# Kernel optimization log

Measured on AMD Instinct MI355X. Metric: run time of the kernel, lower is better.

## Reference

```python
import jax, jax.numpy as jnp
import numpy as np
from jax import lax

B, L, C, P = 512, 6, 4, 45

def _conv(x, w, b, pad):
    y = lax.conv_general_dilated(x, w, (1, 1), [(pad, pad), (pad, pad)],
                                 dimension_numbers=('NCHW', 'OIHW', 'NCHW'))
    return y + b[None, :, None, None]

def _maxpool2(x):
    return lax.reduce_window(x, -jnp.inf, lax.max, (1, 1, 2, 2), (1, 1, 2, 2), 'VALID')

def _prelu(x, a):
    return jnp.where(x >= 0, x, a * x)

def setup_inputs() -> dict:
    key = jax.random.key(0)
    ks = jax.random.split(key, 16)
    s = 0.05
    inp = {
        'x': jax.random.normal(ks[0], (B, L, C, P, P), jnp.float32),
        'w0': jax.random.normal(ks[1], (32, C, 5, 5), jnp.float32) * s,
        'b0': jnp.zeros((32,), jnp.float32),
        'w1': jax.random.normal(ks[2], (32, 32, 5, 5), jnp.float32) * s,
        'b1': jnp.zeros((32,), jnp.float32),
        'w2': jax.random.normal(ks[3], (64, 32, 4, 4), jnp.float32) * s,
        'b2': jnp.zeros((64,), jnp.float32),
        'w3': jax.random.normal(ks[4], (64, 64, 3, 3), jnp.float32) * s,
        'b3': jnp.zeros((64,), jnp.float32),
        'a0': jnp.float32(0.25), 'a1': jnp.float32(0.25),
        'a2': jnp.float32(0.25), 'a3': jnp.float32(0.25),
        'fc1_w': jax.random.normal(ks[5], (L, 256, 128), jnp.float32) * s,
        'fc1_b': jnp.zeros((L, 128), jnp.float32),
        'a4': jnp.full((L, 1), 0.25, jnp.float32),
        'fc2_w': jax.random.normal(ks[6], (L, 128, 64), jnp.float32) * s,
        'fc2_b': jnp.zeros((L, 64), jnp.float32),
        'a5': jnp.full((L, 1), 0.25, jnp.float32),
        'fc3_w': jax.random.normal(ks[7], (L, 64, 4), jnp.float32) * s,
        'fc3_b': jnp.zeros((L, 4), jnp.float32),
    }
    return inp

def reference(x, w0, b0, w1, b1, w2, b2, w3, b3, a0, a1, a2, a3,
              fc1_w, fc1_b, a4, fc2_w, fc2_b, a5, fc3_w, fc3_b):
    b, l = x.shape[0], x.shape[1]
    # Conv tower shares weights across landmarks -> fold landmark into batch.
    h = x.reshape(b * l, x.shape[2], P, P)
    h = _maxpool2(_prelu(_conv(h, w0, b0, 1), a0))   # (BL,32,21,21)
    h = _maxpool2(_prelu(_conv(h, w1, b1, 1), a1))   # (BL,32,9,9)
    h = _maxpool2(_prelu(_conv(h, w2, b2, 1), a2))   # (BL,64,4,4)
    h = _prelu(_conv(h, w3, b3, 0), a3)              # (BL,64,2,2)
    h = h.reshape(b, l, 256)
    # Per-landmark FC heads as batched GEMMs.
    h = _prelu(jnp.einsum('bli,lio->blo', h, fc1_w) + fc1_b, a4)
    h = _prelu(jnp.einsum('bli,lio->blo', h, fc2_w) + fc2_b, a5)
    out = jnp.einsum('bli,lio->blo', h, fc3_w) + fc3_b   # (B,L,4)
    return out
```

## Files before the change

kernel.cpp:

```cpp
#include <hip/hip_runtime.h>
#include <stdint.h>

typedef _Float16 f16;
typedef _Float16 half8 __attribute__((ext_vector_type(8)));
typedef _Float16 half4 __attribute__((ext_vector_type(4)));
typedef float floatx16 __attribute__((ext_vector_type(16)));

#define NIMG 3072

#define WS_W0T   0
#define WS_W1T   10240
#define WS_W2T   61440
#define WS_W3T   126976
#define WS_FC1T  200704
#define WS_FC2T  593920
#define WS_FC3T  692224
#define WS_H2    720896
#define WS_H3F   16646144

#define Z16 {0.f,0.f,0.f,0.f,0.f,0.f,0.f,0.f,0.f,0.f,0.f,0.f,0.f,0.f,0.f,0.f}

__global__ __launch_bounds__(256) void k_prep(
    const float* __restrict__ w0, const float* __restrict__ w1, const float* __restrict__ w2,
    const float* __restrict__ w3, const float* __restrict__ fc1w, const float* __restrict__ fc2w,
    const float* __restrict__ fc3w,
    f16* __restrict__ w0t, f16* __restrict__ w1t, f16* __restrict__ w2t, f16* __restrict__ w3t,
    f16* __restrict__ fc1t, f16* __restrict__ fc2t, f16* __restrict__ fc3t)
{
  int stride = gridDim.x * blockDim.x;
  int g0 = blockIdx.x * blockDim.x + threadIdx.x;
  for (int i = g0; i < 5120; i += stride) {
    int j = i & 7, co = (i >> 3) & 31, hf = (i >> 8) & 1, ch = (i >> 9) & 1, ky = i >> 10;
    int k = ch * 16 + hf * 8 + j;
    f16 v = (f16)0.f;
    if (k < 20) { int kx = k >> 2, ci = k & 3; v = (f16)w0[((co * 4 + ci) * 5 + ky) * 5 + kx]; }
    w0t[i] = v;
  }
  for (int i = g0; i < 25600; i += stride) {
    int j = i & 7, co = (i >> 3) & 31, hf = (i >> 8) & 1, ch = (i >> 9) & 1, tap = i >> 10;
    int ci = ch * 16 + hf * 8 + j, ky = tap / 5, kx = tap % 5;
    w1t[i] = (f16)w1[((co * 32 + ci) * 5 + ky) * 5 + kx];
  }
  for (int i = g0; i < 32768; i += stride) {
    int j = i & 7, co = (i >> 3) & 31, hf = (i >> 8) & 1, ct = (i >> 9) & 1, ch = (i >> 10) & 1, tap = i >> 11;
    int ci = ch * 16 + hf * 8 + j, cog = ct * 32 + co, ky = tap >> 2, kx = tap & 3;
    w2t[i] = (f16)w2[((cog * 32 + ci) * 4 + ky) * 4 + kx];
  }
  for (int i = g0; i < 36864; i += stride) {
    int j = i & 7, col = (i >> 3) & 31, hf = (i >> 8) & 1, ct = (i >> 9) & 1, c = i >> 10;
    int k = c * 16 + hf * 8 + j, tap = k >> 6, ci = k & 63, co = ct * 32 + col;
    int ky = tap / 3, kx = tap % 3;
    w3t[i] = (f16)w3[((co * 64 + ci) * 3 + ky) * 3 + kx];
  }
  for (int i = g0; i < 196608; i += stride) {
    int j = i & 7, col = (i >> 3) & 31, hf = (i >> 8) & 1, nt = (i >> 9) & 3, c = (i >> 11) & 15, l = i >> 15;
    int k = c * 16 + hf * 8 + j, o = nt * 32 + col;
    fc1t[i] = (f16)fc1w[(l * 256 + k) * 128 + o];
  }
  for (int i = g0; i < 49152; i += stride) {
    int j = i & 7, col = (i >> 3) & 31, hf = (i >> 8) & 1, nt = (i >> 9) & 1, c = (i >> 10) & 7, l = i >> 13;
    int k = c * 16 + hf * 8 + j, o = nt * 32 + col;
    fc2t[i] = (f16)fc2w[(l * 128 + k) * 64 + o];
  }
  for (int i = g0; i < 12288; i += stride) {
    int j = i & 7, col = (i >> 3) & 31, hf = (i >> 8) & 1, c = (i >> 9) & 3, l = i >> 11;
    int k = c * 16 + hf * 8 + j;
    f16 v = (f16)0.f;
    if (col < 4) v = (f16)fc3w[(l * 64 + k) * 4 + col];
    fc3t[i] = v;
  }
}

__global__ __launch_bounds__(512) void k_conv01(
    const float* __restrict__ x,
    const f16* __restrict__ w0t, const float* __restrict__ b0, const float* __restrict__ a0p,
    const f16* __restrict__ w1t, const float* __restrict__ b1, const float* __restrict__ a1p,
    f16* __restrict__ h2g)
{
  __shared__ __align__(16) uint32_t smem_u[16328];
  f16* sh   = (f16*)smem_u;
  f16* s_x  = sh;
  f16* s_h1 = sh + 9776;

  const int n = blockIdx.x, tid = threadIdx.x;
  const int wv = tid >> 6, l = tid & 63;
  const int hf = l >> 5, m = l & 31, dr = m >> 3, dc = m & 7, col = m;
  const float a0 = a0p[0], a1 = a1p[0];
  const float b0c = b0[col], b1c = b1[col];
  const half8* w0t8 = (const half8*)w0t;
  const half8* w1t8 = (const half8*)w1t;

  for (int i = tid; i < 16328; i += 512) smem_u[i] = 0u;
  __syncthreads();
  const float* xin = x + n * 8100;
  for (int i = tid; i < 8100; i += 512) {
    int ci = i / 2025, r = i % 2025;
    int y = r / 45, xx = r % 45;
    s_x[((y + 1) * 52 + (xx + 1)) * 4 + ci] = (f16)xin[i];
  }
  __syncthreads();

  half8 B0[5][2];
  #pragma unroll
  for (int ky = 0; ky < 5; ++ky)
    #pragma unroll
    for (int ch = 0; ch < 2; ++ch)
      B0[ky][ch] = w0t8[(ky * 2 + ch) * 64 + hf * 32 + col];

  const int r0lut0[11] = {0,4,8,12,16,20,24,28,32,36,38};
  for (int t = wv; t < 66; t += 8) {
    int r0 = r0lut0[t / 6], cb = (t % 6) * 8;
    int rowb = r0 + dr, colb = cb + dc;
    const f16* pA0 = s_x + (rowb * 52 + colb + 2 * hf) * 4;
    const f16* pA1 = s_x + (rowb * 52 + colb + 4) * 4;
    floatx16 acc = Z16;
    #pragma unroll
    for (int ky = 0; ky < 5; ++ky) {
      half4 lo = *(const half4*)(pA0 + ky * 208);
      half4 hi = *(const half4*)(pA0 + ky * 208 + 4);
      half8 a0v = __builtin_shufflevector(lo, hi, 0,1,2,3,4,5,6,7);
      acc = __builtin_amdgcn_mfma_f32_32x32x16_f16(a0v, B0[ky][0], acc, 0, 0, 0);
      half8 a1v = {(f16)0,(f16)0,(f16)0,(f16)0,(f16)0,(f16)0,(f16)0,(f16)0};
      if (hf == 0) {
        half4 l1 = *(const half4*)(pA1 + ky * 208);
        a1v[0] = l1[0]; a1v[1] = l1[1]; a1v[2] = l1[2]; a1v[3] = l1[3];
      }
      acc = __builtin_amdgcn_mfma_f32_32x32x16_f16(a1v, B0[ky][1], acc, 0, 0, 0);
    }
    #pragma unroll
    for (int pp = 0; pp < 2; ++pp)
      #pragma unroll
      for (int c2 = 0; c2 < 2; ++c2) {
        float v = fmaxf(fmaxf(acc[8*pp + 2*c2], acc[8*pp + 2*c2 + 1]),
                        fmaxf(acc[8*pp + 4 + 2*c2], acc[8*pp + 4 + 2*c2 + 1]));
        v += b0c; v = (v >= 0.f) ? v : a0 * v;
        int pr = (r0 >> 1) + pp, pc = (cb >> 1) + 2 * hf + c2;
        if (pc < 21) s_h1[((pr + 1) * 26 + (pc + 1)) * 40 + col] = (f16)v;
      }
  }
  __syncthreads();

  const int r0lut1[5] = {0, 4, 8, 12, 14};
  const int cclut[3]  = {0, 8, 14};
  int t0 = wv * 2;
  int t1 = t0 + 1; if (t1 > 14) t1 = 14;
  int r0a = r0lut1[t0 / 3], cca = cclut[t0 % 3];
  int r0b = r0lut1[t1 / 3], ccb = cclut[t1 % 3];
  const f16* pAa = s_h1 + ((r0a + dr) * 26 + cca + dc) * 40 + hf * 8;
  const f16* pAb = s_h1 + ((r0b + dr) * 26 + ccb + dc) * 40 + hf * 8;
  floatx16 accA = Z16;
  floatx16 accB = Z16;
  for (int ky = 0; ky < 5; ++ky) {
    const half8* wb = w1t8 + ky * 640 + hf * 32 + col;
    const f16* qa = pAa + ky * 1040;
    const f16* qb = pAb + ky * 1040;
    #pragma unroll
    for (int kx = 0; kx < 5; ++kx) {
      #pragma unroll
      for (int ch = 0; ch < 2; ++ch) {
        half8 b  = wb[kx * 128 + ch * 64];
        half8 aA = *(const half8*)(qa + kx * 40 + ch * 16);
        half8 aB = *(const half8*)(qb + kx * 40 + ch * 16);
        accA = __builtin_amdgcn_mfma_f32_32x32x16_f16(aA, b, accA, 0, 0, 0);
        accB = __builtin_amdgcn_mfma_f32_32x32x16_f16(aB, b, accB, 0, 0, 0);
      }
    }
  }
  f16* outp = h2g + n * 2592;
  #pragma unroll
  for (int tt = 0; tt < 2; ++tt) {
    const floatx16 acc = tt ? accB : accA;
    int r0 = tt ? r0b : r0a, cc = tt ? ccb : cca;
    #pragma unroll
    for (int pp = 0; pp < 2; ++pp)
      #pragma unroll
      for (int c2 = 0; c2 < 2; ++c2) {
        float v = fmaxf(fmaxf(acc[8*pp + 2*c2], acc[8*pp + 2*c2 + 1]),
                        fmaxf(acc[8*pp + 4 + 2*c2], acc[8*pp + 4 + 2*c2 + 1]));
        v += b1c; v = (v >= 0.f) ? v : a1 * v;
        int pr = (r0 >> 1) + pp, pc = (cc >> 1) + 2 * hf + c2;
        if (pc < 9) outp[(pr * 9 + pc) * 32 + col] = (f16)v;
      }
  }
}

__global__ __launch_bounds__(256) void k_conv2(
    const f16* __restrict__ h2g, const f16* __restrict__ w2t,
    const float* __restrict__ b2, const float* __restrict__ a2p,
    f16* __restrict__ h3f)
{
  __shared__ __align__(16) uint32_t s_u[5760];
  f16* s2 = (f16*)s_u;
  const int n0 = blockIdx.x * 2, tid = threadIdx.x;
  const int wv = tid >> 6, l = tid & 63;
  const int hf = l >> 5, m = l & 31, dr = m >> 3, dc = m & 7, col = m;
  const int img = wv >> 1, ct = wv & 1;
  const float a2 = a2p[0];
  const float b2c = b2[ct * 32 + col];
  const half8* w2t8 = (const half8*)w2t;

  for (int i = tid; i < 5760; i += 256) s_u[i] = 0u;
  __syncthreads();
  for (int c = tid; c < 648; c += 256) {
    int im = c / 324, rr = c % 324, pos = rr >> 2, part = rr & 3;
    int r = pos / 9, cc = pos % 9;
    *(half8*)(s2 + im * 5760 + ((r + 1) * 12 + (cc + 1)) * 40 + part * 8) =
      *(const half8*)(h2g + (n0 + im) * 2592 + pos * 32 + part * 8);
  }
  __syncthreads();

  const f16* sbase = s2 + img * 5760;
  const f16* pA0 = sbase + (dr * 12 + dc) * 40 + hf * 8;
  const f16* pA4 = sbase + ((4 + dr) * 12 + dc) * 40 + hf * 8;
  floatx16 acc0 = Z16;
  floatx16 acc4 = Z16;
  for (int tap = 0; tap < 16; ++tap) {
    int ky = tap >> 2, kx = tap & 3;
    int aoff = (ky * 12 + kx) * 40;
    #pragma unroll
    for (int ch = 0; ch < 2; ++ch) {
      half8 b  = w2t8[tap * 256 + ch * 128 + ct * 64 + hf * 32 + col];
      half8 a0 = *(const half8*)(pA0 + aoff + ch * 16);
      half8 a4 = *(const half8*)(pA4 + aoff + ch * 16);
      acc0 = __builtin_amdgcn_mfma_f32_32x32x16_f16(a0, b, acc0, 0, 0, 0);
      acc4 = __builtin_amdgcn_mfma_f32_32x32x16_f16(a4, b, acc4, 0, 0, 0);
    }
  }
  f16* o = h3f + (n0 + img) * 1024;
  #pragma unroll
  for (int tt = 0; tt < 2; ++tt) {
    const floatx16 acc = tt ? acc4 : acc0;
    #pragma unroll
    for (int pp = 0; pp < 2; ++pp)
      #pragma unroll
      for (int c2 = 0; c2 < 2; ++c2) {
        float v = fmaxf(fmaxf(acc[8*pp + 2*c2], acc[8*pp + 2*c2 + 1]),
                        fmaxf(acc[8*pp + 4 + 2*c2], acc[8*pp + 4 + 2*c2 + 1]));
        v += b2c; v = (v >= 0.f) ? v : a2 * v;
        int pr = tt * 2 + pp, pc = 2 * hf + c2, co = ct * 32 + col;
        o[(pr * 4 + pc) * 64 + co] = (f16)v;
      }
  }
}

__global__ __launch_bounds__(256) void k_tail(
    const f16* __restrict__ h3f,
    const f16* __restrict__ w3t, const float* __restrict__ b3, const float* __restrict__ a3p,
    const f16* __restrict__ fc1t, const float* __restrict__ fc1b, const float* __restrict__ a4,
    const f16* __restrict__ fc2t, const float* __restrict__ fc2b, const float* __restrict__ a5,
    const f16* __restrict__ fc3t, const float* __restrict__ fc3b,
    float* __restrict__ out)
{
  __shared__ __align__(16) f16 s_feat[32 * 264];
  __shared__ __align__(16) f16 s_g1[32 * 136];
  __shared__ __align__(16) f16 s_g2[32 * 72];

  const int lm = blockIdx.x % 6, t = blockIdx.x / 6;
  const int tid = threadIdx.x, wv = tid >> 6, lane = tid & 63;
  const int hf = lane >> 5, col = lane & 31;
  const half8* w3t8  = (const half8*)w3t;
  const half8* fc1t8 = (const half8*)fc1t;
  const half8* fc2t8 = (const half8*)fc2t;
  const half8* fc3t8 = (const half8*)fc3t;

  {
    const int mt = wv;
    const int i_img = mt * 8 + (col >> 2);
    const int pos = col & 3, oy = pos >> 1, ox = pos & 1;
    const int gimg = (t * 32 + i_img) * 6 + lm;
    const f16* Abase = h3f + gimg * 1024 + (oy * 4 + ox) * 64;
    floatx16 acc0 = Z16, acc1 = Z16;
    for (int c = 0; c < 36; ++c) {
      int tap = c >> 2;
      int ky = tap / 3, kx = tap % 3;
      half8 a = *(const half8*)(Abase + (ky * 4 + kx) * 64 + (c & 3) * 16 + hf * 8);
      half8 bb0 = w3t8[((c * 2 + 0) * 2 + hf) * 32 + col];
      half8 bb1 = w3t8[((c * 2 + 1) * 2 + hf) * 32 + col];
      acc0 = __builtin_amdgcn_mfma_f32_32x32x16_f16(a, bb0, acc0, 0, 0, 0);
      acc1 = __builtin_amdgcn_mfma_f32_32x32x16_f16(a, bb1, acc1, 0, 0, 0);
    }
    const float a3 = a3p[0];
    #pragma unroll
    for (int ct = 0; ct < 2; ++ct) {
      const floatx16 acc = ct ? acc1 : acc0;
      const int co = ct * 32 + col;
      const float bb = b3[co];
      #pragma unroll
      for (int q = 0; q < 4; ++q) {
        int ii = mt * 8 + 2 * q + hf;
        half4 w;
        #pragma unroll
        for (int z = 0; z < 4; ++z) {
          float v = acc[q * 4 + z] + bb;
          v = (v >= 0.f) ? v : a3 * v;
          w[z] = (f16)v;
        }
        *(half4*)(s_feat + ii * 264 + co * 4) = w;
      }
    }
  }
  __syncthreads();

  {
    floatx16 g = Z16;
    for (int c = 0; c < 16; ++c) {
      half8 a = *(const half8*)(s_feat + col * 264 + c * 16 + hf * 8);
      half8 b = fc1t8[(((lm * 16 + c) * 4 + wv) * 2 + hf) * 32 + col];
      g = __builtin_amdgcn_mfma_f32_32x32x16_f16(a, b, g, 0, 0, 0);
    }
    const float a4v = a4[lm];
    const float bb = fc1b[lm * 128 + wv * 32 + col];
    #pragma unroll
    for (int reg = 0; reg < 16; ++reg) {
      int r = (reg & 3) + 8 * (reg >> 2) + 4 * hf;
      float v = g[reg] + bb;
      v = (v >= 0.f) ? v : a4v * v;
      s_g1[r * 136 + wv * 32 + col] = (f16)v;
    }
  }
  __syncthreads();

  if (wv < 2) {
    floatx16 g = Z16;
    for (int c = 0; c < 8; ++c) {
      half8 a = *(const half8*)(s_g1 + col * 136 + c * 16 + hf * 8);
      half8 b = fc2t8[(((lm * 8 + c) * 2 + wv) * 2 + hf) * 32 + col];
      g = __builtin_amdgcn_mfma_f32_32x32x16_f16(a, b, g, 0, 0, 0);
    }
    const float a5v = a5[lm];
    const float bb = fc2b[lm * 64 + wv * 32 + col];
    #pragma unroll
    for (int reg = 0; reg < 16; ++reg) {
      int r = (reg & 3) + 8 * (reg >> 2) + 4 * hf;
      float v = g[reg] + bb;
      v = (v >= 0.f) ? v : a5v * v;
      s_g2[r * 72 + wv * 32 + col] = (f16)v;
    }
  }
  __syncthreads();

  if (wv == 0) {
    floatx16 g = Z16;
    for (int c = 0; c < 4; ++c) {
      half8 a = *(const half8*)(s_g2 + col * 72 + c * 16 + hf * 8);
      half8 b = fc3t8[((lm * 4 + c) * 2 + hf) * 32 + col];
      g = __builtin_amdgcn_mfma_f32_32x32x16_f16(a, b, g, 0, 0, 0);
    }
    if (col < 4) {
      const float bb = fc3b[lm * 4 + col];
      #pragma unroll
      for (int reg = 0; reg < 16; ++reg) {
        int r = (reg & 3) + 8 * (reg >> 2) + 4 * hf;
        out[((t * 32 + r) * 6 + lm) * 4 + col] = g[reg] + bb;
      }
    }
  }
}

extern "C" void kernel_launch(void* const* d_in, const int* in_sizes, int n_in,
                              void* d_out, int out_size, void* d_ws, size_t ws_size,
                              hipStream_t stream) {
  const float* x    = (const float*)d_in[0];
  const float* w0   = (const float*)d_in[1];
  const float* b0   = (const float*)d_in[2];
  const float* w1   = (const float*)d_in[3];
  const float* b1   = (const float*)d_in[4];
  const float* w2   = (const float*)d_in[5];
  const float* b2   = (const float*)d_in[6];
  const float* w3   = (const float*)d_in[7];
  const float* b3   = (const float*)d_in[8];
  const float* a0   = (const float*)d_in[9];
  const float* a1   = (const float*)d_in[10];
  const float* a2   = (const float*)d_in[11];
  const float* a3   = (const float*)d_in[12];
  const float* fc1w = (const float*)d_in[13];
  const float* fc1b = (const float*)d_in[14];
  const float* a4   = (const float*)d_in[15];
  const float* fc2w = (const float*)d_in[16];
  const float* fc2b = (const float*)d_in[17];
  const float* a5   = (const float*)d_in[18];
  const float* fc3w = (const float*)d_in[19];
  const float* fc3b = (const float*)d_in[20];
  float* out = (float*)d_out;

  char* ws = (char*)d_ws;
  f16* w0t  = (f16*)(ws + WS_W0T);
  f16* w1t  = (f16*)(ws + WS_W1T);
  f16* w2t  = (f16*)(ws + WS_W2T);
  f16* w3t  = (f16*)(ws + WS_W3T);
  f16* fc1t = (f16*)(ws + WS_FC1T);
  f16* fc2t = (f16*)(ws + WS_FC2T);
  f16* fc3t = (f16*)(ws + WS_FC3T);
  f16* h2g  = (f16*)(ws + WS_H2);
  f16* h3f  = (f16*)(ws + WS_H3F);

  k_prep  <<<128, 256, 0, stream>>>(w0, w1, w2, w3, fc1w, fc2w, fc3w,
                                    w0t, w1t, w2t, w3t, fc1t, fc2t, fc3t);
  k_conv01<<<NIMG, 512, 0, stream>>>(x, w0t, b0, a0, w1t, b1, a1, h2g);
  k_conv2 <<<NIMG/2, 256, 0, stream>>>(h2g, w2t, b2, a2, h3f);
  k_tail  <<<96, 256, 0, stream>>>(h3f, w3t, b3, a3, fc1t, fc1b, a4,
                                   fc2t, fc2b, a5, fc3t, fc3b, out);
}
```

Baseline: 336.5 us.

## Split fused conv0/conv1 kernel into separate kernels with global intermediate

Splits the fused conv0+conv1 kernel into two kernels that pass the pooled conv0 activations through a large workspace buffer, with smaller LDS footprints and launch bounds chosen for higher occupancy. conv1 writes its output in place over its own h1 slot, so it adds a __syncthreads before the store. conv0's input padding widens to 56 so the second MFMA operand becomes an unconditional half8 load instead of a zero-filled branch. The fused path stays as a fallback when the workspace is too small. The split adds roughly 87 MB of f16 global write and read traffic for h1 in exchange for better occupancy and the simpler inner loop.

```diff
diff --git a/kernel.cpp b/kernel.cpp
--- a/kernel.cpp
+++ b/kernel.cpp
@@ -15,8 +15,11 @@
 #define WS_FC1T  200704
 #define WS_FC2T  593920
 #define WS_FC3T  692224
-#define WS_H2    720896
-#define WS_H3F   16646144
+#define WS_BIG   720896
+#define H1_BYTES 86704128ull
+#define WS_H3F_FUSED 16646144ull
+#define WS_H3F_SPLIT (720896ull + 86704128ull)
+#define NEED_SPLIT   (WS_H3F_SPLIT + 6291456ull)
 
 #define Z16 {0.f,0.f,0.f,0.f,0.f,0.f,0.f,0.f,0.f,0.f,0.f,0.f,0.f,0.f,0.f,0.f}
 
@@ -71,32 +74,27 @@
   }
 }
 
-__global__ __launch_bounds__(512) void k_conv01(
+__global__ __launch_bounds__(256, 6) void k_conv0(
     const float* __restrict__ x,
     const f16* __restrict__ w0t, const float* __restrict__ b0, const float* __restrict__ a0p,
-    const f16* __restrict__ w1t, const float* __restrict__ b1, const float* __restrict__ a1p,
-    f16* __restrict__ h2g)
+    f16* __restrict__ h1g)
 {
-  __shared__ __align__(16) uint32_t smem_u[16328];
-  f16* sh   = (f16*)smem_u;
-  f16* s_x  = sh;
-  f16* s_h1 = sh + 9776;
-
+  __shared__ __align__(16) uint32_t s_u[5264];
+  f16* s_x = (f16*)s_u;
   const int n = blockIdx.x, tid = threadIdx.x;
   const int wv = tid >> 6, l = tid & 63;
   const int hf = l >> 5, m = l & 31, dr = m >> 3, dc = m & 7, col = m;
-  const float a0 = a0p[0], a1 = a1p[0];
-  const float b0c = b0[col], b1c = b1[col];
+  const float a0 = a0p[0];
+  const float b0c = b0[col];
   const half8* w0t8 = (const half8*)w0t;
-  const half8* w1t8 = (const half8*)w1t;
-
-  for (int i = tid; i < 16328; i += 512) smem_u[i] = 0u;
+
+  for (int i = tid; i < 5264; i += 256) s_u[i] = 0u;
   __syncthreads();
   const float* xin = x + n * 8100;
-  for (int i = tid; i < 8100; i += 512) {
+  for (int i = tid; i < 8100; i += 256) {
     int ci = i / 2025, r = i % 2025;
     int y = r / 45, xx = r % 45;
-    s_x[((y + 1) * 52 + (xx + 1)) * 4 + ci] = (f16)xin[i];
+    s_x[((y + 1) * 56 + (xx + 1)) * 4 + ci] = (f16)xin[i];
   }
   __syncthreads();
 
@@ -108,35 +106,60 @@
       B0[ky][ch] = w0t8[(ky * 2 + ch) * 64 + hf * 32 + col];
 
   const int r0lut0[11] = {0,4,8,12,16,20,24,28,32,36,38};
-  for (int t = wv; t < 66; t += 8) {
+  f16* outb = h1g + n * 14112;
+  for (int t = wv; t < 66; t += 4) {
     int r0 = r0lut0[t / 6], cb = (t % 6) * 8;
     int rowb = r0 + dr, colb = cb + dc;
-    const f16* pA0 = s_x + (rowb * 52 + colb + 2 * hf) * 4;
-    const f16* pA1 = s_x + (rowb * 52 + colb + 4) * 4;
+    const f16* pA = s_x + (rowb * 56 + colb + 2 * hf) * 4;
     floatx16 acc = Z16;
     #pragma unroll
     for (int ky = 0; ky < 5; ++ky) {
-      half4 lo = *(const half4*)(pA0 + ky * 208);
-      half4 hi = *(const half4*)(pA0 + ky * 208 + 4);
-      half8 a0v = __builtin_shufflevector(lo, hi, 0,1,2,3,4,5,6,7);
+      const f16* p = pA + ky * 224;
+      half4 l0  = *(const half4*)(p);
+      half4 h0  = *(const half4*)(p + 4);
+      half4 l1  = *(const half4*)(p + 16);
+      half4 h1v = *(const half4*)(p + 20);
+      half8 a0v = __builtin_shufflevector(l0, h0, 0,1,2,3,4,5,6,7);
+      half8 a1v = __builtin_shufflevector(l1, h1v, 0,1,2,3,4,5,6,7);
       acc = __builtin_amdgcn_mfma_f32_32x32x16_f16(a0v, B0[ky][0], acc, 0, 0, 0);
-      half8 a1v = {(f16)0,(f16)0,(f16)0,(f16)0,(f16)0,(f16)0,(f16)0,(f16)0};
-      if (hf == 0) {
-        half4 l1 = *(const half4*)(pA1 + ky * 208);
-        a1v[0] = l1[0]; a1v[1] = l1[1]; a1v[2] = l1[2]; a1v[3] = l1[3];
-      }
       acc = __builtin_amdgcn_mfma_f32_32x32x16_f16(a1v, B0[ky][1], acc, 0, 0, 0);
     }
     #pragma unroll
     for (int pp = 0; pp < 2; ++pp)
       #pragma unroll
       for (int c2 = 0; c2 < 2; ++c2) {
-        float v = fmaxf(fmaxf(acc[8*pp + 2*c2], acc[8*pp + 2*c2 + 1]),
-                        fmaxf(acc[8*pp + 4 + 2*c2], acc[8*pp + 4 + 2*c2 + 1]));
-        v += b0c; v = (v >= 0.f) ? v : a0 * v;
+        float mm = fmaxf(fmaxf(acc[8*pp + 2*c2], acc[8*pp + 2*c2 + 1]),
+                         fmaxf(acc[8*pp + 4 + 2*c2], acc[8*pp + 4 + 2*c2 + 1]));
+        mm += b0c;
+        float v = fmaxf(mm, 0.f) + a0 * fminf(mm, 0.f);
         int pr = (r0 >> 1) + pp, pc = (cb >> 1) + 2 * hf + c2;
-        if (pc < 21) s_h1[((pr + 1) * 26 + (pc + 1)) * 40 + col] = (f16)v;
-      }
+        if (pc < 21) outb[(pr * 21 + pc) * 32 + col] = (f16)v;
+      }
+  }
+}
+
+__global__ __launch_bounds__(512, 6) void k_conv1(
+    const f16* __restrict__ h1g,
+    const f16* __restrict__ w1t, const float* __restrict__ b1, const float* __restrict__ a1p,
+    f16* __restrict__ h2g, int h2stride)
+{
+  __shared__ __align__(16) uint32_t s_u[11440];
+  f16* s_h1 = (f16*)s_u;
+  const int n = blockIdx.x, tid = threadIdx.x;
+  const int wv = tid >> 6, l = tid & 63;
+  const int hf = l >> 5, m = l & 31, dr = m >> 3, dc = m & 7, col = m;
+  const float a1 = a1p[0];
+  const float b1c = b1[col];
+  const half8* w1t8 = (const half8*)w1t;
+
+  for (int i = tid; i < 11440; i += 512) s_u[i] = 0u;
+  __syncthreads();
+  const f16* inb = h1g + n * 14112;
+  for (int i = tid; i < 1764; i += 512) {
+    int pos = i >> 2, part = i & 3;
+    int r = pos / 21, c = pos % 21;
+    *(half8*)(s_h1 + ((r + 1) * 26 + (c + 1)) * 40 + part * 8) =
+      *(const half8*)(inb + pos * 32 + part * 8);
   }
   __syncthreads();
 
@@ -166,7 +189,8 @@
       }
     }
   }
-  f16* outp = h2g + n * 2592;
+  __syncthreads();
+  f16* outp = h2g + n * h2stride;
   #pragma unroll
   for (int tt = 0; tt < 2; ++tt) {
     const floatx16 acc = tt ? accB : accA;
@@ -184,8 +208,121 @@
   }
 }
 
+__global__ __launch_bounds__(512) void k_conv01(
+    const float* __restrict__ x,
+    const f16* __restrict__ w0t, const float* __restrict__ b0, const float* __restrict__ a0p,
+    const f16* __restrict__ w1t, const float* __restrict__ b1, const float* __restrict__ a1p,
+    f16* __restrict__ h2g)
+{
+  __shared__ __align__(16) uint32_t smem_u[16328];
+  f16* sh   = (f16*)smem_u;
+  f16* s_x  = sh;
+  f16* s_h1 = sh + 9776;
+
+  const int n = blockIdx.x, tid = threadIdx.x;
+  const int wv = tid >> 6, l = tid & 63;
+  const int hf = l >> 5, m = l & 31, dr = m >> 3, dc = m & 7, col = m;
+  const float a0 = a0p[0], a1 = a1p[0];
+  const float b0c = b0[col], b1c = b1[col];
+  const half8* w0t8 = (const half8*)w0t;
+  const half8* w1t8 = (const half8*)w1t;
+
+  for (int i = tid; i < 16328; i += 512) smem_u[i] = 0u;
+  __syncthreads();
+  const float* xin = x + n * 8100;
+  for (int i = tid; i < 8100; i += 512) {
+    int ci = i / 2025, r = i % 2025;
+    int y = r / 45, xx = r % 45;
+    s_x[((y + 1) * 52 + (xx + 1)) * 4 + ci] = (f16)xin[i];
+  }
+  __syncthreads();
+
+  half8 B0[5][2];
+  #pragma unroll
+  for (int ky = 0; ky < 5; ++ky)
+    #pragma unroll
+    for (int ch = 0; ch < 2; ++ch)
+      B0[ky][ch] = w0t8[(ky * 2 + ch) * 64 + hf * 32 + col];
+
+  const int r0lut0[11] = {0,4,8,12,16,20,24,28,32,36,38};
+  for (int t = wv; t < 66; t += 8) {
+    int r0 = r0lut0[t / 6], cb = (t % 6) * 8;
+    int rowb = r0 + dr, colb = cb + dc;
+    const f16* pA0 = s_x + (rowb * 52 + colb + 2 * hf) * 4;
+    const f16* pA1 = s_x + (rowb * 52 + colb + 4) * 4;
+    floatx16 acc = Z16;
+    #pragma unroll
+    for (int ky = 0; ky < 5; ++ky) {
+      half4 lo = *(const half4*)(pA0 + ky * 208);
+      half4 hi = *(const half4*)(pA0 + ky * 208 + 4);
+      half8 a0v = __builtin_shufflevector(lo, hi, 0,1,2,3,4,5,6,7);
+      acc = __builtin_amdgcn_mfma_f32_32x32x16_f16(a0v, B0[ky][0], acc, 0, 0, 0);
+      half8 a1v = {(f16)0,(f16)0,(f16)0,(f16)0,(f16)0,(f16)0,(f16)0,(f16)0};
+      if (hf == 0) {
+        half4 l1 = *(const half4*)(pA1 + ky * 208);
+        a1v[0] = l1[0]; a1v[1] = l1[1]; a1v[2] = l1[2]; a1v[3] = l1[3];
+      }
+      acc = __builtin_amdgcn_mfma_f32_32x32x16_f16(a1v, B0[ky][1], acc, 0, 0, 0);
+    }
+    #pragma unroll
+    for (int pp = 0; pp < 2; ++pp)
+      #pragma unroll
+      for (int c2 = 0; c2 < 2; ++c2) {
+        float v = fmaxf(fmaxf(acc[8*pp + 2*c2], acc[8*pp + 2*c2 + 1]),
+                        fmaxf(acc[8*pp + 4 + 2*c2], acc[8*pp + 4 + 2*c2 + 1]));
+        v += b0c; v = (v >= 0.f) ? v : a0 * v;
+        int pr = (r0 >> 1) + pp, pc = (cb >> 1) + 2 * hf + c2;
+        if (pc < 21) s_h1[((pr + 1) * 26 + (pc + 1)) * 40 + col] = (f16)v;
+      }
+  }
+  __syncthreads();
+
+  const int r0lut1[5] = {0, 4, 8, 12, 14};
+  const int cclut[3]  = {0, 8, 14};
+  int t0 = wv * 2;
+  int t1 = t0 + 1; if (t1 > 14) t1 = 14;
+  int r0a = r0lut1[t0 / 3], cca = cclut[t0 % 3];
+  int r0b = r0lut1[t1 / 3], ccb = cclut[t1 % 3];
+  const f16* pAa = s_h1 + ((r0a + dr) * 26 + cca + dc) * 40 + hf * 8;
+  const f16* pAb = s_h1 + ((r0b + dr) * 26 + ccb + dc) * 40 + hf * 8;
+  floatx16 accA = Z16;
+  floatx16 accB = Z16;
+  for (int ky = 0; ky < 5; ++ky) {
+    const half8* wb = w1t8 + ky * 640 + hf * 32 + col;
+    const f16* qa = pAa + ky * 1040;
+    const f16* qb = pAb + ky * 1040;
+    #pragma unroll
+    for (int kx = 0; kx < 5; ++kx) {
+      #pragma unroll
+      for (int ch = 0; ch < 2; ++ch) {
+        half8 b  = wb[kx * 128 + ch * 64];
+        half8 aA = *(const half8*)(qa + kx * 40 + ch * 16);
+        half8 aB = *(const half8*)(qb + kx * 40 + ch * 16);
+        accA = __builtin_amdgcn_mfma_f32_32x32x16_f16(aA, b, accA, 0, 0, 0);
+        accB = __builtin_amdgcn_mfma_f32_32x32x16_f16(aB, b, accB, 0, 0, 0);
+      }
+    }
+  }
+  f16* outp = h2g + n * 2592;
+  #pragma unroll
+  for (int tt = 0; tt < 2; ++tt) {
+    const floatx16 acc = tt ? accB : accA;
+    int r0 = tt ? r0b : r0a, cc = tt ? ccb : cca;
+    #pragma unroll
+    for (int pp = 0; pp < 2; ++pp)
+      #pragma unroll
+      for (int c2 = 0; c2 < 2; ++c2) {
+        float v = fmaxf(fmaxf(acc[8*pp + 2*c2], acc[8*pp + 2*c2 + 1]),
+                        fmaxf(acc[8*pp + 4 + 2*c2], acc[8*pp + 4 + 2*c2 + 1]));
+        v += b1c; v = (v >= 0.f) ? v : a1 * v;
+        int pr = (r0 >> 1) + pp, pc = (cc >> 1) + 2 * hf + c2;
+        if (pc < 9) outp[(pr * 9 + pc) * 32 + col] = (f16)v;
+      }
+  }
+}
+
 __global__ __launch_bounds__(256) void k_conv2(
-    const f16* __restrict__ h2g, const f16* __restrict__ w2t,
+    const f16* __restrict__ h2g, int h2stride, const f16* __restrict__ w2t,
     const float* __restrict__ b2, const float* __restrict__ a2p,
     f16* __restrict__ h3f)
 {
@@ -205,7 +342,7 @@
     int im = c / 324, rr = c % 324, pos = rr >> 2, part = rr & 3;
     int r = pos / 9, cc = pos % 9;
     *(half8*)(s2 + im * 5760 + ((r + 1) * 12 + (cc + 1)) * 40 + part * 8) =
-      *(const half8*)(h2g + (n0 + im) * 2592 + pos * 32 + part * 8);
+      *(const half8*)(h2g + (size_t)(n0 + im) * h2stride + pos * 32 + part * 8);
   }
   __syncthreads();
 
@@ -391,13 +528,24 @@
   f16* fc1t = (f16*)(ws + WS_FC1T);
   f16* fc2t = (f16*)(ws + WS_FC2T);
   f16* fc3t = (f16*)(ws + WS_FC3T);
-  f16* h2g  = (f16*)(ws + WS_H2);
-  f16* h3f  = (f16*)(ws + WS_H3F);
-
-  k_prep  <<<128, 256, 0, stream>>>(w0, w1, w2, w3, fc1w, fc2w, fc3w,
-                                    w0t, w1t, w2t, w3t, fc1t, fc2t, fc3t);
-  k_conv01<<<NIMG, 512, 0, stream>>>(x, w0t, b0, a0, w1t, b1, a1, h2g);
-  k_conv2 <<<NIMG/2, 256, 0, stream>>>(h2g, w2t, b2, a2, h3f);
-  k_tail  <<<96, 256, 0, stream>>>(h3f, w3t, b3, a3, fc1t, fc1b, a4,
-                                   fc2t, fc2b, a5, fc3t, fc3b, out);
-}
+
+  k_prep<<<128, 256, 0, stream>>>(w0, w1, w2, w3, fc1w, fc2w, fc3w,
+                                  w0t, w1t, w2t, w3t, fc1t, fc2t, fc3t);
+
+  if (ws_size >= NEED_SPLIT) {
+    f16* h1  = (f16*)(ws + WS_BIG);
+    f16* h3f = (f16*)(ws + WS_H3F_SPLIT);
+    k_conv0<<<NIMG, 256, 0, stream>>>(x, w0t, b0, a0, h1);
+    k_conv1<<<NIMG, 512, 0, stream>>>(h1, w1t, b1, a1, h1, 14112);
+    k_conv2<<<NIMG/2, 256, 0, stream>>>(h1, 14112, w2t, b2, a2, h3f);
+    k_tail <<<96, 256, 0, stream>>>(h3f, w3t, b3, a3, fc1t, fc1b, a4,
+                                    fc2t, fc2b, a5, fc3t, fc3b, out);
+  } else {
+    f16* h2g = (f16*)(ws + WS_BIG);
+    f16* h3f = (f16*)(ws + WS_H3F_FUSED);
+    k_conv01<<<NIMG, 512, 0, stream>>>(x, w0t, b0, a0, w1t, b1, a1, h2g);
+    k_conv2 <<<NIMG/2, 256, 0, stream>>>(h2g, 2592, w2t, b2, a2, h3f);
+    k_tail  <<<96, 256, 0, stream>>>(h3f, w3t, b3, a3, fc1t, fc1b, a4,
+                                     fc2t, fc2b, a5, fc3t, fc3b, out);
+  }
+}
```

Measured after the change: 349.1 us. 3.7% more time.

## Fuse conv2 into conv01 kernel, keeping conv1 output in shared memory

Applied to the files above, without the earlier changes.

Merges the third convolution stage into the per-image conv0/conv1 kernel, so pooled conv1 activations stay in LDS instead of going to global memory and being read back by a separate kernel. This drops one launch and the global round trip for the intermediate. The conv0 input padding stride grows from 52 to 56, so the second K-chunk can be loaded without the hf branch and zero fill. Conv2 now runs on only 2 of the 8 waves per block, leaving the rest idle, and LDS use rises slightly, which may reduce occupancy.

```diff
diff --git a/kernel.cpp b/kernel.cpp
--- a/kernel.cpp
+++ b/kernel.cpp
@@ -15,8 +15,7 @@
 #define WS_FC1T  200704
 #define WS_FC2T  593920
 #define WS_FC3T  692224
-#define WS_H2    720896
-#define WS_H3F   16646144
+#define WS_H3F   720896
 
 #define Z16 {0.f,0.f,0.f,0.f,0.f,0.f,0.f,0.f,0.f,0.f,0.f,0.f,0.f,0.f,0.f,0.f}
 
@@ -71,16 +70,18 @@
   }
 }
 
-__global__ __launch_bounds__(512) void k_conv01(
+__global__ __launch_bounds__(512) void k_conv012(
     const float* __restrict__ x,
     const f16* __restrict__ w0t, const float* __restrict__ b0, const float* __restrict__ a0p,
     const f16* __restrict__ w1t, const float* __restrict__ b1, const float* __restrict__ a1p,
-    f16* __restrict__ h2g)
+    const f16* __restrict__ w2t, const float* __restrict__ b2, const float* __restrict__ a2p,
+    f16* __restrict__ h3f)
 {
-  __shared__ __align__(16) uint32_t smem_u[16328];
+  __shared__ __align__(16) uint32_t smem_u[16704];
   f16* sh   = (f16*)smem_u;
   f16* s_x  = sh;
-  f16* s_h1 = sh + 9776;
+  f16* s_h1 = sh + 10528;
+  f16* s_h2 = sh;
 
   const int n = blockIdx.x, tid = threadIdx.x;
   const int wv = tid >> 6, l = tid & 63;
@@ -89,14 +90,15 @@
   const float b0c = b0[col], b1c = b1[col];
   const half8* w0t8 = (const half8*)w0t;
   const half8* w1t8 = (const half8*)w1t;
-
-  for (int i = tid; i < 16328; i += 512) smem_u[i] = 0u;
+  const half8* w2t8 = (const half8*)w2t;
+
+  for (int i = tid; i < 16704; i += 512) smem_u[i] = 0u;
   __syncthreads();
   const float* xin = x + n * 8100;
   for (int i = tid; i < 8100; i += 512) {
     int ci = i / 2025, r = i % 2025;
     int y = r / 45, xx = r % 45;
-    s_x[((y + 1) * 52 + (xx + 1)) * 4 + ci] = (f16)xin[i];
+    s_x[((y + 1) * 56 + (xx + 1)) * 4 + ci] = (f16)xin[i];
   }
   __syncthreads();
 
@@ -111,20 +113,18 @@
   for (int t = wv; t < 66; t += 8) {
     int r0 = r0lut0[t / 6], cb = (t % 6) * 8;
     int rowb = r0 + dr, colb = cb + dc;
-    const f16* pA0 = s_x + (rowb * 52 + colb + 2 * hf) * 4;
-    const f16* pA1 = s_x + (rowb * 52 + colb + 4) * 4;
+    const f16* pA = s_x + (rowb * 56 + colb + 2 * hf) * 4;
     floatx16 acc = Z16;
     #pragma unroll
     for (int ky = 0; ky < 5; ++ky) {
-      half4 lo = *(const half4*)(pA0 + ky * 208);
-      half4 hi = *(const half4*)(pA0 + ky * 208 + 4);
-      half8 a0v = __builtin_shufflevector(lo, hi, 0,1,2,3,4,5,6,7);
+      const f16* p = pA + ky * 224;
+      half4 l0  = *(const half4*)(p);
+      half4 h0  = *(const half4*)(p + 4);
+      half4 l1  = *(const half4*)(p + 16);
+      half4 h1v = *(const half4*)(p + 20);
+      half8 a0v = __builtin_shufflevector(l0, h0, 0,1,2,3,4,5,6,7);
+      half8 a1v = __builtin_shufflevector(l1, h1v, 0,1,2,3,4,5,6,7);
       acc = __builtin_amdgcn_mfma_f32_32x32x16_f16(a0v, B0[ky][0], acc, 0, 0, 0);
-      half8 a1v = {(f16)0,(f16)0,(f16)0,(f16)0,(f16)0,(f16)0,(f16)0,(f16)0};
-      if (hf == 0) {
-        half4 l1 = *(const half4*)(pA1 + ky * 208);
-        a1v[0] = l1[0]; a1v[1] = l1[1]; a1v[2] = l1[2]; a1v[3] = l1[3];
-      }
       acc = __builtin_amdgcn_mfma_f32_32x32x16_f16(a1v, B0[ky][1], acc, 0, 0, 0);
     }
     #pragma unroll
@@ -138,6 +138,9 @@
         if (pc < 21) s_h1[((pr + 1) * 26 + (pc + 1)) * 40 + col] = (f16)v;
       }
   }
+  __syncthreads();
+
+  for (int i = tid; i < 2880; i += 512) smem_u[i] = 0u;
   __syncthreads();
 
   const int r0lut1[5] = {0, 4, 8, 12, 14};
@@ -166,7 +169,6 @@
       }
     }
   }
-  f16* outp = h2g + n * 2592;
   #pragma unroll
   for (int tt = 0; tt < 2; ++tt) {
     const floatx16 acc = tt ? accB : accA;
@@ -179,67 +181,46 @@
                         fmaxf(acc[8*pp + 4 + 2*c2], acc[8*pp + 4 + 2*c2 + 1]));
         v += b1c; v = (v >= 0.f) ? v : a1 * v;
         int pr = (r0 >> 1) + pp, pc = (cc >> 1) + 2 * hf + c2;
-        if (pc < 9) outp[(pr * 9 + pc) * 32 + col] = (f16)v;
-      }
-  }
-}
-
-__global__ __launch_bounds__(256) void k_conv2(
-    const f16* __restrict__ h2g, const f16* __restrict__ w2t,
-    const float* __restrict__ b2, const float* __restrict__ a2p,
-    f16* __restrict__ h3f)
-{
-  __shared__ __align__(16) uint32_t s_u[5760];
-  f16* s2 = (f16*)s_u;
-  const int n0 = blockIdx.x * 2, tid = threadIdx.x;
-  const int wv = tid >> 6, l = tid & 63;
-  const int hf = l >> 5, m = l & 31, dr = m >> 3, dc = m & 7, col = m;
-  const int img = wv >> 1, ct = wv & 1;
-  const float a2 = a2p[0];
-  const float b2c = b2[ct * 32 + col];
-  const half8* w2t8 = (const half8*)w2t;
-
-  for (int i = tid; i < 5760; i += 256) s_u[i] = 0u;
-  __syncthreads();
-  for (int c = tid; c < 648; c += 256) {
-    int im = c / 324, rr = c % 324, pos = rr >> 2, part = rr & 3;
-    int r = pos / 9, cc = pos % 9;
-    *(half8*)(s2 + im * 5760 + ((r + 1) * 12 + (cc + 1)) * 40 + part * 8) =
-      *(const half8*)(h2g + (n0 + im) * 2592 + pos * 32 + part * 8);
-  }
-  __syncthreads();
-
-  const f16* sbase = s2 + img * 5760;
-  const f16* pA0 = sbase + (dr * 12 + dc) * 40 + hf * 8;
-  const f16* pA4 = sbase + ((4 + dr) * 12 + dc) * 40 + hf * 8;
-  floatx16 acc0 = Z16;
-  floatx16 acc4 = Z16;
-  for (int tap = 0; tap < 16; ++tap) {
-    int ky = tap >> 2, kx = tap & 3;
-    int aoff = (ky * 12 + kx) * 40;
-    #pragma unroll
-    for (int ch = 0; ch < 2; ++ch) {
-      half8 b  = w2t8[tap * 256 + ch * 128 + ct * 64 + hf * 32 + col];
-      half8 a0 = *(const half8*)(pA0 + aoff + ch * 16);
-      half8 a4 = *(const half8*)(pA4 + aoff + ch * 16);
-      acc0 = __builtin_amdgcn_mfma_f32_32x32x16_f16(a0, b, acc0, 0, 0, 0);
-      acc4 = __builtin_amdgcn_mfma_f32_32x32x16_f16(a4, b, acc4, 0, 0, 0);
-    }
-  }
-  f16* o = h3f + (n0 + img) * 1024;
-  #pragma unroll
-  for (int tt = 0; tt < 2; ++tt) {
-    const floatx16 acc = tt ? acc4 : acc0;
-    #pragma unroll
-    for (int pp = 0; pp < 2; ++pp)
-      #pragma unroll
-      for (int c2 = 0; c2 < 2; ++c2) {
-        float v = fmaxf(fmaxf(acc[8*pp + 2*c2], acc[8*pp + 2*c2 + 1]),
-                        fmaxf(acc[8*pp + 4 + 2*c2], acc[8*pp + 4 + 2*c2 + 1]));
-        v += b2c; v = (v >= 0.f) ? v : a2 * v;
-        int pr = tt * 2 + pp, pc = 2 * hf + c2, co = ct * 32 + col;
-        o[(pr * 4 + pc) * 64 + co] = (f16)v;
-      }
+        if (pc < 9) s_h2[((pr + 1) * 12 + (pc + 1)) * 40 + col] = (f16)v;
+      }
+  }
+  __syncthreads();
+
+  if (wv < 2) {
+    const int ct = wv;
+    const float a2 = a2p[0];
+    const float b2c = b2[ct * 32 + col];
+    const f16* pA0 = s_h2 + (dr * 12 + dc) * 40 + hf * 8;
+    const f16* pA4 = s_h2 + ((4 + dr) * 12 + dc) * 40 + hf * 8;
+    floatx16 acc0 = Z16;
+    floatx16 acc4 = Z16;
+    for (int tap = 0; tap < 16; ++tap) {
+      int ky = tap >> 2, kx = tap & 3;
+      int aoff = (ky * 12 + kx) * 40;
+      #pragma unroll
+      for (int ch = 0; ch < 2; ++ch) {
+        half8 b  = w2t8[tap * 256 + ch * 128 + ct * 64 + hf * 32 + col];
+        half8 a0v = *(const half8*)(pA0 + aoff + ch * 16);
+        half8 a4v = *(const half8*)(pA4 + aoff + ch * 16);
+        acc0 = __builtin_amdgcn_mfma_f32_32x32x16_f16(a0v, b, acc0, 0, 0, 0);
+        acc4 = __builtin_amdgcn_mfma_f32_32x32x16_f16(a4v, b, acc4, 0, 0, 0);
+      }
+    }
+    f16* o = h3f + n * 1024;
+    #pragma unroll
+    for (int tt = 0; tt < 2; ++tt) {
+      const floatx16 acc = tt ? acc4 : acc0;
+      #pragma unroll
+      for (int pp = 0; pp < 2; ++pp)
+        #pragma unroll
+        for (int c2 = 0; c2 < 2; ++c2) {
+          float v = fmaxf(fmaxf(acc[8*pp + 2*c2], acc[8*pp + 2*c2 + 1]),
+                          fmaxf(acc[8*pp + 4 + 2*c2], acc[8*pp + 4 + 2*c2 + 1]));
+          v += b2c; v = (v >= 0.f) ? v : a2 * v;
+          int pr = tt * 2 + pp, pc = 2 * hf + c2, co = ct * 32 + col;
+          o[(pr * 4 + pc) * 64 + co] = (f16)v;
+        }
+    }
   }
 }
 
@@ -391,13 +372,11 @@
   f16* fc1t = (f16*)(ws + WS_FC1T);
   f16* fc2t = (f16*)(ws + WS_FC2T);
   f16* fc3t = (f16*)(ws + WS_FC3T);
-  f16* h2g  = (f16*)(ws + WS_H2);
   f16* h3f  = (f16*)(ws + WS_H3F);
 
-  k_prep  <<<128, 256, 0, stream>>>(w0, w1, w2, w3, fc1w, fc2w, fc3w,
-                                    w0t, w1t, w2t, w3t, fc1t, fc2t, fc3t);
-  k_conv01<<<NIMG, 512, 0, stream>>>(x, w0t, b0, a0, w1t, b1, a1, h2g);
-  k_conv2 <<<NIMG/2, 256, 0, stream>>>(h2g, w2t, b2, a2, h3f);
-  k_tail  <<<96, 256, 0, stream>>>(h3f, w3t, b3, a3, fc1t, fc1b, a4,
-                                   fc2t, fc2b, a5, fc3t, fc3b, out);
+  k_prep   <<<128, 256, 0, stream>>>(w0, w1, w2, w3, fc1w, fc2w, fc3w,
+                                     w0t, w1t, w2t, w3t, fc1t, fc2t, fc3t);
+  k_conv012<<<NIMG, 512, 0, stream>>>(x, w0t, b0, a0, w1t, b1, a1, w2t, b2, a2, h3f);
+  k_tail   <<<96, 256, 0, stream>>>(h3f, w3t, b3, a3, fc1t, fc1b, a4,
+                                    fc2t, fc2b, a5, fc3t, fc3b, out);
 }
```

After: 338.9 us. About the same (+0.7%).
